# Kernel tuning notes

Measured on AMD Instinct MI355X. Metric: run time of the kernel, lower is better.

Reference implementation:

```python
import jax, jax.numpy as jnp
import numpy as np

N, E, R, H, FDIM, OUT = 50000, 800000, 12, 128, 1582, 2
Q = H // 4  # 32
SLOPE = 0.01  # LeakyReLU default negative slope


def leaky(x):
    return jnp.where(x > 0, x, SLOPE * x)


def rgcn(x, src, dst, etype, W, root, bias):
    # Per-relation mean aggregation of neighbor features, then linear transform
    # (PyG RGCNConv default aggr='mean'). Linear => transform-then-mean is equal.
    # count of edges of each (relation, dst) pair
    seg = etype * N + dst
    cnt = jnp.zeros((R * N,), x.dtype).at[seg].add(1.0)
    norm = 1.0 / jnp.maximum(cnt[seg], 1.0)          # [E]
    xw = jnp.einsum('nh,rhd->nrd', x, W)             # [N,R,H] per-relation transform
    msg = xw[src, etype] * norm[:, None]             # [E,H] gather + normalize
    agg = jax.ops.segment_sum(msg, dst, num_segments=N)  # [N,H] scatter-add
    return agg + x @ root + bias


def setup_inputs() -> dict:
    key = jax.random.key(0)
    ks = jax.random.split(key, 16)
    s = lambda d: 1.0 / np.sqrt(d)
    inp = {
        'feature': jax.random.normal(ks[0], (N, FDIM), jnp.float32),
        'edge_index': jax.random.randint(ks[1], (2, E), 0, N),
        'edge_type': jax.random.randint(ks[2], (E,), 0, R),
        'W_des': jax.random.normal(ks[3], (768, Q), jnp.float32) * s(768),
        'b_des': jnp.zeros((Q,), jnp.float32),
        'W_tweet': jax.random.normal(ks[4], (768, Q), jnp.float32) * s(768),
        'b_tweet': jnp.zeros((Q,), jnp.float32),
        'W_num': jax.random.normal(ks[5], (34, Q), jnp.float32) * s(34),
        'b_num': jnp.zeros((Q,), jnp.float32),
        'W_cat': jax.random.normal(ks[6], (12, Q), jnp.float32) * s(12),
        'b_cat': jnp.zeros((Q,), jnp.float32),
        'W_in': jax.random.normal(ks[7], (H, H), jnp.float32) * s(H),
        'b_in': jnp.zeros((H,), jnp.float32),
        'rgcn_W': jax.random.normal(ks[8], (R, H, H), jnp.float32) * s(H),
        'rgcn_root': jax.random.normal(ks[9], (H, H), jnp.float32) * s(H),
        'rgcn_bias': jnp.zeros((H,), jnp.float32),
        'W_out1': jax.random.normal(ks[10], (H, H), jnp.float32) * s(H),
        'b_out1': jnp.zeros((H,), jnp.float32),
        'W_out2': jax.random.normal(ks[11], (H, OUT), jnp.float32) * s(H),
        'b_out2': jnp.zeros((OUT,), jnp.float32),
    }
    return inp


def reference(feature, edge_index, edge_type, W_des, b_des, W_tweet, b_tweet,
              W_num, b_num, W_cat, b_cat, W_in, b_in, rgcn_W, rgcn_root,
              rgcn_bias, W_out1, b_out1, W_out2, b_out2):
    src, dst = edge_index[0], edge_index[1]
    d = leaky(feature[:, -1536:-768] @ W_des + b_des)
    t = leaky(feature[:, -768:] @ W_tweet + b_tweet)
    num = leaky(feature[:, 12:46] @ W_num + b_num)
    cat = leaky(feature[:, 0:12] @ W_cat + b_cat)
    x = jnp.concatenate((d, t, num, cat), axis=1)       # [N,H]
    x = leaky(x @ W_in + b_in)
    x = rgcn(x, src, dst, edge_type, rgcn_W, rgcn_root, rgcn_bias)
    # dropout: identity in eval mode (deterministic reference)
    x = rgcn(x, src, dst, edge_type, rgcn_W, rgcn_root, rgcn_bias)
    x = leaky(x @ W_out1 + b_out1)
    return x @ W_out2 + b_out2
```

## Files before the change

kernel.cpp:

```cpp
#include <hip/hip_runtime.h>
#include <stdint.h>

#define NN 50000
#define NE 800000
#define NR 12
#define NRX 13
#define NH 128
#define NF 1582
#define NSEG (NN * NR)
#define MT 3125
#define MT2 1563
#define SCAN_NB ((NSEG + 255) / 256)
#define KSENC 50
#define CTXW (NRX * 8)

typedef __attribute__((ext_vector_type(8))) short short8;
typedef __attribute__((ext_vector_type(4))) float floatx4;

__device__ __forceinline__ float bf2f(unsigned int u16) {
    union { unsigned int i; float f; } w; w.i = u16 << 16; return w.f;
}
__device__ __forceinline__ unsigned short f2bf(float f) {
    union { float f; unsigned int i; } w; w.f = f;
    unsigned int i = w.i;
    return (unsigned short)((i + 0x7FFFu + ((i >> 16) & 1u)) >> 16);
}
__device__ __forceinline__ float leaky_f(float v) { return v > 0.f ? v : 0.01f * v; }
__device__ __forceinline__ float fast_rcp(float x) {
    float r; asm("v_rcp_f32 %0, %1" : "=v"(r) : "v"(x)); return r;
}

__global__ __launch_bounds__(256) void swz_k(
    const float* __restrict__ src1, int K1,
    const float* __restrict__ src2, int Ktot, int N, int KS,
    unsigned short* __restrict__ dst)
{
    const int idx = blockIdx.x * 256 + threadIdx.x;
    const int total = (N >> 4) * KS * 512;
    if (idx >= total) return;
    const int j = idx & 7;
    const int lane = (idx >> 3) & 63;
    const int cks = idx >> 9;
    const int ks = cks % KS;
    const int ct = cks / KS;
    const int k = ks * 32 + (lane >> 4) * 8 + j;
    const int col = ct * 16 + (lane & 15);
    float v = 0.f;
    if (k < Ktot) v = (k < K1) ? src1[(size_t)k * N + col] : src2[(size_t)(k - K1) * N + col];
    dst[idx] = f2bf(v);
}

__global__ __launch_bounds__(256) void swzxw_k(
    const float* __restrict__ rgW, const float* __restrict__ root,
    unsigned short* __restrict__ dst)
{
    const int idx = blockIdx.x * 256 + threadIdx.x;
    const int total = CTXW * 4 * 512;
    if (idx >= total) return;
    const int j = idx & 7;
    const int lane = (idx >> 3) & 63;
    const int cks = idx >> 9;
    const int ks = cks & 3;
    const int ctg = cks >> 2;
    const int r = ctg >> 3;
    const int ct8 = ctg & 7;
    const int k = ks * 32 + (lane >> 4) * 8 + j;
    const int c = ct8 * 16 + (lane & 15);
    const float v = (r < NR) ? rgW[((size_t)r * NH + k) * NH + c]
                             : root[(size_t)k * NH + c];
    dst[idx] = f2bf(v);
}

__global__ __launch_bounds__(256) void swzenc_k(
    const float* __restrict__ Wdes, const float* __restrict__ Wtw,
    const float* __restrict__ Wnum, const float* __restrict__ Wcat,
    unsigned short* __restrict__ dst)
{
    const int idx = blockIdx.x * 256 + threadIdx.x;
    const int total = 8 * KSENC * 512;
    if (idx >= total) return;
    const int j = idx & 7;
    const int lane = (idx >> 3) & 63;
    const int cks = idx >> 9;
    const int ks = cks % KSENC;
    const int ct = cks / KSENC;
    const int k = ks * 32 + (lane >> 4) * 8 + j;
    const int col = ct * 16 + (lane & 15);
    float v = 0.f;
    if (col < 32) {
        if (k >= 46 && k < 814)   v = Wdes[(size_t)(k - 46) * 32 + col];
    } else if (col < 64) {
        if (k >= 814 && k < 1582) v = Wtw[(size_t)(k - 814) * 32 + (col - 32)];
    } else if (col < 96) {
        if (k >= 12 && k < 46)    v = Wnum[(size_t)(k - 12) * 32 + (col - 64)];
    } else {
        if (k < 12)               v = Wcat[(size_t)k * 32 + (col - 96)];
    }
    dst[idx] = f2bf(v);
}

__global__ __launch_bounds__(128) void packbias_k(
    const float* __restrict__ bdes, const float* __restrict__ btw,
    const float* __restrict__ bnum, const float* __restrict__ bcat,
    float* __restrict__ be)
{
    const int c = threadIdx.x;
    float v;
    if (c < 32) v = bdes[c];
    else if (c < 64) v = btw[c - 32];
    else if (c < 96) v = bnum[c - 64];
    else v = bcat[c - 96];
    be[c] = v;
}

__global__ __launch_bounds__(256) void hist_k(const int* __restrict__ dst,
                                              const int* __restrict__ et,
                                              int* __restrict__ deg)
{
    const int e = blockIdx.x * 256 + threadIdx.x;
    if (e >= NE) return;
    atomicAdd(&deg[dst[e] * NR + et[e]], 1);
}

__global__ __launch_bounds__(256) void scanA_k(const int* __restrict__ deg,
                                               int* __restrict__ offs,
                                               int* __restrict__ part)
{
    __shared__ int lds[256];
    const int i = blockIdx.x * 256 + threadIdx.x;
    const int v = (i < NSEG) ? deg[i] : 0;
    lds[threadIdx.x] = v; __syncthreads();
#pragma unroll
    for (int d = 1; d < 256; d <<= 1) {
        const int t = (threadIdx.x >= d) ? lds[threadIdx.x - d] : 0;
        __syncthreads();
        lds[threadIdx.x] += t;
        __syncthreads();
    }
    if (i < NSEG) offs[i] = lds[threadIdx.x] - v;
    if (threadIdx.x == 255) part[blockIdx.x] = lds[255];
}

__global__ __launch_bounds__(256) void scanB_k(int* __restrict__ part, int nb)
{
    __shared__ int lds[256];
    __shared__ int carry;
    if (threadIdx.x == 0) carry = 0;
    __syncthreads();
    for (int base = 0; base < nb; base += 256) {
        const int i = base + threadIdx.x;
        const int v = (i < nb) ? part[i] : 0;
        lds[threadIdx.x] = v; __syncthreads();
#pragma unroll
        for (int d = 1; d < 256; d <<= 1) {
            const int t = (threadIdx.x >= d) ? lds[threadIdx.x - d] : 0;
            __syncthreads();
            lds[threadIdx.x] += t;
            __syncthreads();
        }
        if (i < nb) part[i] = lds[threadIdx.x] - v + carry;
        __syncthreads();
        if (threadIdx.x == 255) carry += lds[255];
        __syncthreads();
    }
}

__global__ __launch_bounds__(256) void scanC_k(int* __restrict__ offs,
                                               const int* __restrict__ part)
{
    const int i = blockIdx.x * 256 + threadIdx.x;
    if (i < NSEG) offs[i] += part[blockIdx.x];
}

__global__ __launch_bounds__(256) void fill_k(const int* __restrict__ src,
                                              const int* __restrict__ dst,
                                              const int* __restrict__ et,
                                              const int* __restrict__ offs,
                                              const int* __restrict__ deg,
                                              int* __restrict__ cur,
                                              unsigned int* __restrict__ eidx)
{
    const int e = blockIdx.x * 256 + threadIdx.x;
    if (e >= NE) return;
    const int r = et[e];
    const int s = dst[e] * NR + r;
    const int pos = offs[s] + atomicAdd(&cur[s], 1);
    int n = deg[s]; if (n > 4095) n = 4095;
    eidx[pos] = (unsigned int)(src[e] * NRX + r) | ((unsigned int)n << 20);
}

__global__ __launch_bounds__(256) void enc_k(
    const float* __restrict__ feat,
    const unsigned short* __restrict__ Benc, const float* __restrict__ be,
    const unsigned short* __restrict__ Bwin, const float* __restrict__ bin,
    unsigned short* __restrict__ xa)
{
    const int wave = threadIdx.x >> 6, lane = threadIdx.x & 63;
    const int q = lane >> 4, cl = lane & 15;
    int tile = blockIdx.x * 4 + wave;
    if (tile >= MT) tile = MT - 1;
    const int row = tile * 16 + cl;

    const int lo[8] = {1, 1, 25, 25, 0, 0, 0, 0};
    const int hi[8] = {26, 26, 50, 50, 2, 2, 1, 1};

    floatx4 acc[8];
#pragma unroll
    for (int ct = 0; ct < 8; ct++) { floatx4 z = {0.f,0.f,0.f,0.f}; acc[ct] = z; }

    for (int ks = 0; ks < KSENC; ks++) {
        const int kb = ks * 32 + q * 8;
        union { short8 v; unsigned short u[8]; } a;
        const float* ap = feat + (size_t)row * NF + kb;
        if (kb + 7 < NF) {
#pragma unroll
            for (int j = 0; j < 4; j++) {
                const float2 t = *(const float2*)__builtin_assume_aligned(ap + 2 * j, 8);
                a.u[2 * j]     = f2bf(t.x);
                a.u[2 * j + 1] = f2bf(t.y);
            }
        } else {
#pragma unroll
            for (int j = 0; j < 8; j++)
                a.u[j] = ((kb + j) < NF) ? f2bf(ap[j]) : 0;
        }
#pragma unroll
        for (int ct = 0; ct < 8; ct++) {
            if (ks >= lo[ct] && ks < hi[ct]) {
                const short8 b = *(const short8*)(Benc + ((size_t)(ct * KSENC + ks) * 64 + lane) * 8);
                acc[ct] = __builtin_amdgcn_mfma_f32_16x16x32_bf16(a.v, b, acc[ct], 0, 0, 0);
            }
        }
    }

    __shared__ unsigned short lds[4][16][136];
#pragma unroll
    for (int ct = 0; ct < 8; ct++) {
        const int col = ct * 16 + cl;
        const float bv = be[col];
#pragma unroll
        for (int r = 0; r < 4; r++)
            lds[wave][q * 4 + r][col] = f2bf(leaky_f(acc[ct][r] + bv));
    }
    __syncthreads();

    floatx4 acc2[8];
#pragma unroll
    for (int ct = 0; ct < 8; ct++) { floatx4 z = {0.f,0.f,0.f,0.f}; acc2[ct] = z; }
#pragma unroll
    for (int ks2 = 0; ks2 < 4; ks2++) {
        const short8 a2 = *(const short8*)&lds[wave][cl][ks2 * 32 + q * 8];
#pragma unroll
        for (int ct = 0; ct < 8; ct++) {
            const short8 b = *(const short8*)(Bwin + ((size_t)(ct * 4 + ks2) * 64 + lane) * 8);
            acc2[ct] = __builtin_amdgcn_mfma_f32_16x16x32_bf16(a2, b, acc2[ct], 0, 0, 0);
        }
    }
#pragma unroll
    for (int ct = 0; ct < 8; ct++) {
        const int col = ct * 16 + cl;
        const float bv = bin[col];
#pragma unroll
        for (int r = 0; r < 4; r++)
            xa[(size_t)(tile * 16 + q * 4 + r) * NH + col] = f2bf(leaky_f(acc2[ct][r] + bv));
    }
}

__global__ __launch_bounds__(256) void xw_k(
    const unsigned short* __restrict__ xin,
    const unsigned short* __restrict__ Bxw,
    unsigned short* __restrict__ xw)
{
    const int wave = threadIdx.x >> 6, lane = threadIdx.x & 63;
    const int q = lane >> 4, cl = lane & 15;
    int wid = blockIdx.x * 4 + wave;
    if (wid >= MT2 * NRX) wid = MT2 * NRX - 1;
    __shared__ unsigned short tl[4][2][16][136];
    const int t2 = wid / NRX;
    const int r = wid - t2 * NRX;
    const int ta = t2 * 2;
    const int tb = (ta + 1 < MT) ? ta + 1 : MT - 1;

    floatx4 accA[8], accB[8];
#pragma unroll
    for (int ct = 0; ct < 8; ct++) {
        floatx4 z = {0.f,0.f,0.f,0.f}; accA[ct] = z; accB[ct] = z;
    }
#pragma unroll
    for (int ks = 0; ks < 4; ks++) {
        const short8 aA = *(const short8*)__builtin_assume_aligned(
            xin + (size_t)(ta * 16 + cl) * NH + ks * 32 + q * 8, 16);
        const short8 aB = *(const short8*)__builtin_assume_aligned(
            xin + (size_t)(tb * 16 + cl) * NH + ks * 32 + q * 8, 16);
#pragma unroll
        for (int ct = 0; ct < 8; ct++) {
            const short8 b = *(const short8*)(Bxw + ((size_t)((r * 8 + ct) * 4 + ks) * 64 + lane) * 8);
            accA[ct] = __builtin_amdgcn_mfma_f32_16x16x32_bf16(aA, b, accA[ct], 0, 0, 0);
            accB[ct] = __builtin_amdgcn_mfma_f32_16x16x32_bf16(aB, b, accB[ct], 0, 0, 0);
        }
    }
#pragma unroll
    for (int ct = 0; ct < 8; ct++) {
        const int col = ct * 16 + cl;
#pragma unroll
        for (int rr = 0; rr < 4; rr++) {
            tl[wave][0][q * 4 + rr][col] = f2bf(accA[ct][rr]);
            tl[wave][1][q * 4 + rr][col] = f2bf(accB[ct][rr]);
        }
    }
    __syncthreads();
#pragma unroll
    for (int i = 0; i < 4; i++) {
        const int row = i * 4 + q;
        const short8 vA = *(const short8*)&tl[wave][0][row][cl * 8];
        const short8 vB = *(const short8*)&tl[wave][1][row][cl * 8];
        *(short8*)(xw + ((size_t)(ta * 16 + row) * NRX + r) * NH + cl * 8) = vA;
        *(short8*)(xw + ((size_t)(tb * 16 + row) * NRX + r) * NH + cl * 8) = vB;
    }
}

#define ACC8(fk, tv, wv) \
    fk[0] += (wv) * bf2f((tv).x & 0xFFFFu); fk[1] += (wv) * bf2f((tv).x >> 16); \
    fk[2] += (wv) * bf2f((tv).y & 0xFFFFu); fk[3] += (wv) * bf2f((tv).y >> 16); \
    fk[4] += (wv) * bf2f((tv).z & 0xFFFFu); fk[5] += (wv) * bf2f((tv).z >> 16); \
    fk[6] += (wv) * bf2f((tv).w & 0xFFFFu); fk[7] += (wv) * bf2f((tv).w >> 16);

#define INIT8(fk, tv) \
    fk[0] = bf2f((tv).x & 0xFFFFu); fk[1] = bf2f((tv).x >> 16); \
    fk[2] = bf2f((tv).y & 0xFFFFu); fk[3] = bf2f((tv).y >> 16); \
    fk[4] = bf2f((tv).z & 0xFFFFu); fk[5] = bf2f((tv).z >> 16); \
    fk[6] = bf2f((tv).w & 0xFFFFu); fk[7] = bf2f((tv).w >> 16);

__global__ __launch_bounds__(256) void gather_k(
    const unsigned short* __restrict__ xw,
    const unsigned int* __restrict__ eidx,
    const int* __restrict__ offs,
    const float* __restrict__ rbias,
    unsigned short* __restrict__ xout)
{
    const int wave = threadIdx.x >> 6, lane = threadIdx.x & 63;
    const int q = lane >> 4, cl = lane & 15;
    const int wid = blockIdx.x * 4 + wave;
    const int tile = wid >> 1;
    if (tile >= MT) return;
    const int half = wid & 1;
    const int cA = half * 8 + q;
    const int cB = cA + 4;
    const int d = tile * 16 + cl;
    const int beg = offs[d * NR];
    const int end = (d < NN - 1) ? offs[(d + 1) * NR] : NE;

    float fA[8], fB[8];
    {
        const unsigned short* xr = xw + ((size_t)d * NRX + NR) * NH;
        const uint4 tA = *(const uint4*)(xr + cA * 8);
        const uint4 tB = *(const uint4*)(xr + cB * 8);
        INIT8(fA, tA); INIT8(fB, tB);
    }

    for (int e = beg; e < end; e += 2) {
        const int e1 = (e + 1 < end) ? e + 1 : e;
        const unsigned int v0 = eidx[e];
        const unsigned int v1 = eidx[e1];
        const float w0 = fast_rcp((float)(v0 >> 20));
        const float w1 = (e + 1 < end) ? fast_rcp((float)(v1 >> 20)) : 0.f;
        const unsigned short* x0 = xw + (size_t)(v0 & 0xFFFFFu) * NH;
        const unsigned short* x1 = xw + (size_t)(v1 & 0xFFFFFu) * NH;
        const uint4 a0 = *(const uint4*)(x0 + cA * 8);
        const uint4 b0 = *(const uint4*)(x0 + cB * 8);
        const uint4 a1 = *(const uint4*)(x1 + cA * 8);
        const uint4 b1 = *(const uint4*)(x1 + cB * 8);
        ACC8(fA, a0, w0); ACC8(fB, b0, w0);
        ACC8(fA, a1, w1); ACC8(fB, b1, w1);
    }

    union { short8 v; unsigned short u[8]; } oA, oB;
#pragma unroll
    for (int m = 0; m < 8; m++) {
        oA.u[m] = f2bf(fA[m] + rbias[cA * 8 + m]);
        oB.u[m] = f2bf(fB[m] + rbias[cB * 8 + m]);
    }
    *(short8*)(xout + (size_t)d * NH + cA * 8) = oA.v;
    *(short8*)(xout + (size_t)d * NH + cB * 8) = oB.v;
}

__global__ __launch_bounds__(256) void head_k(
    const unsigned short* __restrict__ xa,
    const unsigned short* __restrict__ Bo1, const float* __restrict__ bo1,
    const float* __restrict__ Wo2, const float* __restrict__ bo2,
    float* __restrict__ out)
{
    const int wave = threadIdx.x >> 6, lane = threadIdx.x & 63;
    const int q = lane >> 4, cl = lane & 15;
    int tile = blockIdx.x * 4 + wave;
    if (tile >= MT) tile = MT - 1;

    floatx4 acc[8];
#pragma unroll
    for (int ct = 0; ct < 8; ct++) { floatx4 z = {0.f,0.f,0.f,0.f}; acc[ct] = z; }
#pragma unroll
    for (int ks = 0; ks < 4; ks++) {
        const short8 a = *(const short8*)__builtin_assume_aligned(
            xa + (size_t)(tile * 16 + cl) * NH + ks * 32 + q * 8, 16);
#pragma unroll
        for (int ct = 0; ct < 8; ct++) {
            const short8 b = *(const short8*)(Bo1 + ((size_t)(ct * 4 + ks) * 64 + lane) * 8);
            acc[ct] = __builtin_amdgcn_mfma_f32_16x16x32_bf16(a, b, acc[ct], 0, 0, 0);
        }
    }
    __shared__ unsigned short lds[4][16][136];
#pragma unroll
    for (int ct = 0; ct < 8; ct++) {
        const int col = ct * 16 + cl;
        const float bv = bo1[col];
#pragma unroll
        for (int r = 0; r < 4; r++)
            lds[wave][q * 4 + r][col] = f2bf(leaky_f(acc[ct][r] + bv));
    }
    __syncthreads();

    if (lane < 32) {
        const int row = lane >> 1, o = lane & 1;
        float s = bo2[o];
        for (int k = 0; k < NH; k++)
            s += bf2f(lds[wave][row][k]) * Wo2[k * 2 + o];
        out[(size_t)(tile * 16 + row) * 2 + o] = s;
    }
}

extern "C" void kernel_launch(void* const* d_in, const int* in_sizes, int n_in,
                              void* d_out, int out_size, void* d_ws, size_t ws_size,
                              hipStream_t stream)
{
    const float* feat = (const float*)d_in[0];
    const int* ei   = (const int*)d_in[1];
    const int* et   = (const int*)d_in[2];
    const float* Wdes = (const float*)d_in[3];
    const float* bdes = (const float*)d_in[4];
    const float* Wtw  = (const float*)d_in[5];
    const float* btw  = (const float*)d_in[6];
    const float* Wnum = (const float*)d_in[7];
    const float* bnum = (const float*)d_in[8];
    const float* Wcat = (const float*)d_in[9];
    const float* bcat = (const float*)d_in[10];
    const float* Win  = (const float*)d_in[11];
    const float* bin  = (const float*)d_in[12];
    const float* rgW  = (const float*)d_in[13];
    const float* root = (const float*)d_in[14];
    const float* rbias= (const float*)d_in[15];
    const float* Wo1  = (const float*)d_in[16];
    const float* bo1  = (const float*)d_in[17];
    const float* Wo2  = (const float*)d_in[18];
    const float* bo2  = (const float*)d_in[19];
    const int* srcp = ei;
    const int* dstp = ei + NE;

    char* p = (char*)d_ws;
    auto alloc = [&](size_t bytes) { char* r = p; p += (bytes + 255) & ~(size_t)255; return r; };
    unsigned short* xa = (unsigned short*)alloc((size_t)NN * NH * 2);
    unsigned short* xb = (unsigned short*)alloc((size_t)NN * NH * 2);
    int* deg  = (int*)alloc((size_t)NSEG * 4);
    int* offs = (int*)alloc((size_t)NSEG * 4);
    int* cur  = (int*)alloc((size_t)NSEG * 4);
    int* part = (int*)alloc((size_t)(SCAN_NB + 8) * 4);
    unsigned int* eidx = (unsigned int*)alloc((size_t)NE * 4);
    unsigned short* Benc = (unsigned short*)alloc((size_t)8 * KSENC * 512 * 2);
    unsigned short* sWin = (unsigned short*)alloc((size_t)8 * 4 * 512 * 2);
    unsigned short* Bxw  = (unsigned short*)alloc((size_t)CTXW * 4 * 512 * 2);
    unsigned short* sWo1 = (unsigned short*)alloc((size_t)8 * 4 * 512 * 2);
    float* be = (float*)alloc(128 * 4);
    unsigned short* xwbuf = (unsigned short*)alloc((size_t)NN * NRX * NH * 2);

    const int GB = (MT + 3) / 4;
    const int GBXW = (MT2 * NRX + 3) / 4;
    const int GB2 = (MT * 2 + 3) / 4;

    hipMemsetAsync(deg, 0, (size_t)NSEG * 4, stream);
    hipMemsetAsync(cur, 0, (size_t)NSEG * 4, stream);
    hist_k<<<(NE + 255) / 256, 256, 0, stream>>>(dstp, et, deg);
    scanA_k<<<SCAN_NB, 256, 0, stream>>>(deg, offs, part);
    scanB_k<<<1, 256, 0, stream>>>(part, SCAN_NB);
    scanC_k<<<SCAN_NB, 256, 0, stream>>>(offs, part);
    fill_k<<<(NE + 255) / 256, 256, 0, stream>>>(srcp, dstp, et, offs, deg, cur, eidx);

    swzenc_k<<<(8 * KSENC * 512 + 255) / 256, 256, 0, stream>>>(Wdes, Wtw, Wnum, Wcat, Benc);
    packbias_k<<<1, 128, 0, stream>>>(bdes, btw, bnum, bcat, be);
    swz_k<<<(8 * 4 * 512 + 255) / 256, 256, 0, stream>>>(Win, 128, Win, 128, 128, 4, sWin);
    swzxw_k<<<(CTXW * 4 * 512 + 255) / 256, 256, 0, stream>>>(rgW, root, Bxw);
    swz_k<<<(8 * 4 * 512 + 255) / 256, 256, 0, stream>>>(Wo1, 128, Wo1, 128, 128, 4, sWo1);

    enc_k<<<GB, 256, 0, stream>>>(feat, Benc, be, sWin, bin, xa);
    xw_k<<<GBXW, 256, 0, stream>>>(xa, Bxw, xwbuf);
    gather_k<<<GB2, 256, 0, stream>>>(xwbuf, eidx, offs, rbias, xb);
    xw_k<<<GBXW, 256, 0, stream>>>(xb, Bxw, xwbuf);
    gather_k<<<GB2, 256, 0, stream>>>(xwbuf, eidx, offs, rbias, xa);
    head_k<<<GB, 256, 0, stream>>>(xa, sWo1, bo1, Wo2, bo2, (float*)d_out);
}
```

Measured before the change: 840.9 us.

## Merge prep kernels, drop scan fixup, fuse head into gather, unroll gather by four

Folds the weight-swizzle and bias-pack kernels into one prep kernel and replaces the memsets with a zero kernel. The scan fixup pass is removed; consumers add the block partial sum on the fly. The output head is fused into the second gather through shared memory, and the gather loop is unrolled to four edges per iteration for more memory-level parallelism. This cuts launch count and global round trips, at the cost of extra registers and a block-wide barrier in gather.

```diff
diff --git a/kernel.cpp b/kernel.cpp
--- a/kernel.cpp
+++ b/kernel.cpp
@@ -13,6 +13,10 @@
 #define SCAN_NB ((NSEG + 255) / 256)
 #define KSENC 50
 #define CTXW (NRX * 8)
+#define TOTENC (8 * KSENC * 512)
+#define TOT128 (8 * 4 * 512)
+#define TOTXW  (CTXW * 4 * 512)
+#define TOTPREP (TOTENC + TOT128 + TOTXW + TOT128 + 128)
 
 typedef __attribute__((ext_vector_type(8))) short short8;
 typedef __attribute__((ext_vector_type(4))) float floatx4;
@@ -30,87 +34,96 @@
     float r; asm("v_rcp_f32 %0, %1" : "=v"(r) : "v"(x)); return r;
 }
 
-__global__ __launch_bounds__(256) void swz_k(
-    const float* __restrict__ src1, int K1,
-    const float* __restrict__ src2, int Ktot, int N, int KS,
-    unsigned short* __restrict__ dst)
-{
-    const int idx = blockIdx.x * 256 + threadIdx.x;
-    const int total = (N >> 4) * KS * 512;
-    if (idx >= total) return;
-    const int j = idx & 7;
-    const int lane = (idx >> 3) & 63;
-    const int cks = idx >> 9;
-    const int ks = cks % KS;
-    const int ct = cks / KS;
-    const int k = ks * 32 + (lane >> 4) * 8 + j;
-    const int col = ct * 16 + (lane & 15);
-    float v = 0.f;
-    if (k < Ktot) v = (k < K1) ? src1[(size_t)k * N + col] : src2[(size_t)(k - K1) * N + col];
-    dst[idx] = f2bf(v);
-}
-
-__global__ __launch_bounds__(256) void swzxw_k(
-    const float* __restrict__ rgW, const float* __restrict__ root,
-    unsigned short* __restrict__ dst)
-{
-    const int idx = blockIdx.x * 256 + threadIdx.x;
-    const int total = CTXW * 4 * 512;
-    if (idx >= total) return;
-    const int j = idx & 7;
-    const int lane = (idx >> 3) & 63;
-    const int cks = idx >> 9;
-    const int ks = cks & 3;
-    const int ctg = cks >> 2;
-    const int r = ctg >> 3;
-    const int ct8 = ctg & 7;
-    const int k = ks * 32 + (lane >> 4) * 8 + j;
-    const int c = ct8 * 16 + (lane & 15);
-    const float v = (r < NR) ? rgW[((size_t)r * NH + k) * NH + c]
-                             : root[(size_t)k * NH + c];
-    dst[idx] = f2bf(v);
-}
-
-__global__ __launch_bounds__(256) void swzenc_k(
+__global__ __launch_bounds__(256) void prep_k(
     const float* __restrict__ Wdes, const float* __restrict__ Wtw,
     const float* __restrict__ Wnum, const float* __restrict__ Wcat,
-    unsigned short* __restrict__ dst)
-{
-    const int idx = blockIdx.x * 256 + threadIdx.x;
-    const int total = 8 * KSENC * 512;
-    if (idx >= total) return;
-    const int j = idx & 7;
-    const int lane = (idx >> 3) & 63;
-    const int cks = idx >> 9;
-    const int ks = cks % KSENC;
-    const int ct = cks / KSENC;
-    const int k = ks * 32 + (lane >> 4) * 8 + j;
-    const int col = ct * 16 + (lane & 15);
-    float v = 0.f;
-    if (col < 32) {
-        if (k >= 46 && k < 814)   v = Wdes[(size_t)(k - 46) * 32 + col];
-    } else if (col < 64) {
-        if (k >= 814 && k < 1582) v = Wtw[(size_t)(k - 814) * 32 + (col - 32)];
-    } else if (col < 96) {
-        if (k >= 12 && k < 46)    v = Wnum[(size_t)(k - 12) * 32 + (col - 64)];
-    } else {
-        if (k < 12)               v = Wcat[(size_t)k * 32 + (col - 96)];
-    }
-    dst[idx] = f2bf(v);
-}
-
-__global__ __launch_bounds__(128) void packbias_k(
+    const float* __restrict__ Win,  const float* __restrict__ rgW,
+    const float* __restrict__ root, const float* __restrict__ Wo1,
     const float* __restrict__ bdes, const float* __restrict__ btw,
     const float* __restrict__ bnum, const float* __restrict__ bcat,
+    unsigned short* __restrict__ Benc, unsigned short* __restrict__ sWin,
+    unsigned short* __restrict__ Bxw,  unsigned short* __restrict__ sWo1,
     float* __restrict__ be)
 {
-    const int c = threadIdx.x;
-    float v;
-    if (c < 32) v = bdes[c];
-    else if (c < 64) v = btw[c - 32];
-    else if (c < 96) v = bnum[c - 64];
-    else v = bcat[c - 96];
-    be[c] = v;
+    int idx = blockIdx.x * 256 + threadIdx.x;
+    if (idx < TOTENC) {
+        const int j = idx & 7;
+        const int lane = (idx >> 3) & 63;
+        const int cks = idx >> 9;
+        const int ks = cks % KSENC;
+        const int ct = cks / KSENC;
+        const int k = ks * 32 + (lane >> 4) * 8 + j;
+        const int col = ct * 16 + (lane & 15);
+        float v = 0.f;
+        if (col < 32) {
+            if (k >= 46 && k < 814)   v = Wdes[(size_t)(k - 46) * 32 + col];
+        } else if (col < 64) {
+            if (k >= 814 && k < 1582) v = Wtw[(size_t)(k - 814) * 32 + (col - 32)];
+        } else if (col < 96) {
+            if (k >= 12 && k < 46)    v = Wnum[(size_t)(k - 12) * 32 + (col - 64)];
+        } else {
+            if (k < 12)               v = Wcat[(size_t)k * 32 + (col - 96)];
+        }
+        Benc[idx] = f2bf(v);
+        return;
+    }
+    idx -= TOTENC;
+    if (idx < TOT128) {
+        const int j = idx & 7;
+        const int lane = (idx >> 3) & 63;
+        const int cks = idx >> 9;
+        const int ks = cks & 3;
+        const int ct = cks >> 2;
+        const int k = ks * 32 + (lane >> 4) * 8 + j;
+        const int col = ct * 16 + (lane & 15);
+        sWin[idx] = f2bf(Win[(size_t)k * NH + col]);
+        return;
+    }
+    idx -= TOT128;
+    if (idx < TOTXW) {
+        const int j = idx & 7;
+        const int lane = (idx >> 3) & 63;
+        const int cks = idx >> 9;
+        const int ks = cks & 3;
+        const int ctg = cks >> 2;
+        const int r = ctg >> 3;
+        const int ct8 = ctg & 7;
+        const int k = ks * 32 + (lane >> 4) * 8 + j;
+        const int c = ct8 * 16 + (lane & 15);
+        const float v = (r < NR) ? rgW[((size_t)r * NH + k) * NH + c]
+                                 : root[(size_t)k * NH + c];
+        Bxw[idx] = f2bf(v);
+        return;
+    }
+    idx -= TOTXW;
+    if (idx < TOT128) {
+        const int j = idx & 7;
+        const int lane = (idx >> 3) & 63;
+        const int cks = idx >> 9;
+        const int ks = cks & 3;
+        const int ct = cks >> 2;
+        const int k = ks * 32 + (lane >> 4) * 8 + j;
+        const int col = ct * 16 + (lane & 15);
+        sWo1[idx] = f2bf(Wo1[(size_t)k * NH + col]);
+        return;
+    }
+    idx -= TOT128;
+    if (idx < 128) {
+        const int c = idx;
+        float v;
+        if (c < 32) v = bdes[c];
+        else if (c < 64) v = btw[c - 32];
+        else if (c < 96) v = bnum[c - 64];
+        else v = bcat[c - 96];
+        be[c] = v;
+    }
+}
+
+__global__ __launch_bounds__(256) void zero_k(int* __restrict__ deg,
+                                              int* __restrict__ cur)
+{
+    const int i = blockIdx.x * 256 + threadIdx.x;
+    if (i < NSEG) { deg[i] = 0; cur[i] = 0; }
 }
 
 __global__ __launch_bounds__(256) void hist_k(const int* __restrict__ dst,
@@ -165,17 +178,11 @@
     }
 }
 
-__global__ __launch_bounds__(256) void scanC_k(int* __restrict__ offs,
-                                               const int* __restrict__ part)
-{
-    const int i = blockIdx.x * 256 + threadIdx.x;
-    if (i < NSEG) offs[i] += part[blockIdx.x];
-}
-
 __global__ __launch_bounds__(256) void fill_k(const int* __restrict__ src,
                                               const int* __restrict__ dst,
                                               const int* __restrict__ et,
                                               const int* __restrict__ offs,
+                                              const int* __restrict__ part,
                                               const int* __restrict__ deg,
                                               int* __restrict__ cur,
                                               unsigned int* __restrict__ eidx)
@@ -184,7 +191,7 @@
     if (e >= NE) return;
     const int r = et[e];
     const int s = dst[e] * NR + r;
-    const int pos = offs[s] + atomicAdd(&cur[s], 1);
+    const int pos = offs[s] + part[s >> 8] + atomicAdd(&cur[s], 1);
     int n = deg[s]; if (n > 4095) n = 4095;
     eidx[pos] = (unsigned int)(src[e] * NRX + r) | ((unsigned int)n << 20);
 }
@@ -334,21 +341,31 @@
 __global__ __launch_bounds__(256) void gather_k(
     const unsigned short* __restrict__ xw,
     const unsigned int* __restrict__ eidx,
-    const int* __restrict__ offs,
+    const int* __restrict__ offs, const int* __restrict__ part,
     const float* __restrict__ rbias,
-    unsigned short* __restrict__ xout)
+    unsigned short* __restrict__ xout,
+    const int do_head,
+    const unsigned short* __restrict__ Bo1, const float* __restrict__ bo1,
+    const float* __restrict__ Wo2, const float* __restrict__ bo2,
+    float* __restrict__ out)
 {
     const int wave = threadIdx.x >> 6, lane = threadIdx.x & 63;
     const int q = lane >> 4, cl = lane & 15;
-    const int wid = blockIdx.x * 4 + wave;
+    int wid = blockIdx.x * 4 + wave;
+    if (wid >= MT * 2) wid = MT * 2 - 1;
     const int tile = wid >> 1;
-    if (tile >= MT) return;
     const int half = wid & 1;
+    const int lt = wave >> 1;
+    __shared__ unsigned short lx[2][16][136];
+
     const int cA = half * 8 + q;
     const int cB = cA + 4;
     const int d = tile * 16 + cl;
-    const int beg = offs[d * NR];
-    const int end = (d < NN - 1) ? offs[(d + 1) * NR] : NE;
+    const int s0 = d * NR;
+    const int beg = offs[s0] + part[s0 >> 8];
+    int end;
+    if (d < NN - 1) { const int s1 = s0 + NR; end = offs[s1] + part[s1 >> 8]; }
+    else end = NE;
 
     float fA[8], fB[8];
     {
@@ -358,20 +375,34 @@
         INIT8(fA, tA); INIT8(fB, tB);
     }
 
-    for (int e = beg; e < end; e += 2) {
+    for (int e = beg; e < end; e += 4) {
         const int e1 = (e + 1 < end) ? e + 1 : e;
+        const int e2 = (e + 2 < end) ? e + 2 : e;
+        const int e3 = (e + 3 < end) ? e + 3 : e;
         const unsigned int v0 = eidx[e];
         const unsigned int v1 = eidx[e1];
+        const unsigned int v2 = eidx[e2];
+        const unsigned int v3 = eidx[e3];
         const float w0 = fast_rcp((float)(v0 >> 20));
         const float w1 = (e + 1 < end) ? fast_rcp((float)(v1 >> 20)) : 0.f;
+        const float w2 = (e + 2 < end) ? fast_rcp((float)(v2 >> 20)) : 0.f;
+        const float w3 = (e + 3 < end) ? fast_rcp((float)(v3 >> 20)) : 0.f;
         const unsigned short* x0 = xw + (size_t)(v0 & 0xFFFFFu) * NH;
         const unsigned short* x1 = xw + (size_t)(v1 & 0xFFFFFu) * NH;
+        const unsigned short* x2 = xw + (size_t)(v2 & 0xFFFFFu) * NH;
+        const unsigned short* x3 = xw + (size_t)(v3 & 0xFFFFFu) * NH;
         const uint4 a0 = *(const uint4*)(x0 + cA * 8);
         const uint4 b0 = *(const uint4*)(x0 + cB * 8);
         const uint4 a1 = *(const uint4*)(x1 + cA * 8);
         const uint4 b1 = *(const uint4*)(x1 + cB * 8);
+        const uint4 a2 = *(const uint4*)(x2 + cA * 8);
+        const uint4 b2 = *(const uint4*)(x2 + cB * 8);
+        const uint4 a3 = *(const uint4*)(x3 + cA * 8);
+        const uint4 b3 = *(const uint4*)(x3 + cB * 8);
         ACC8(fA, a0, w0); ACC8(fB, b0, w0);
         ACC8(fA, a1, w1); ACC8(fB, b1, w1);
+        ACC8(fA, a2, w2); ACC8(fB, b2, w2);
+        ACC8(fA, a3, w3); ACC8(fB, b3, w3);
     }
 
     union { short8 v; unsigned short u[8]; } oA, oB;
@@ -380,51 +411,44 @@
         oA.u[m] = f2bf(fA[m] + rbias[cA * 8 + m]);
         oB.u[m] = f2bf(fB[m] + rbias[cB * 8 + m]);
     }
-    *(short8*)(xout + (size_t)d * NH + cA * 8) = oA.v;
-    *(short8*)(xout + (size_t)d * NH + cB * 8) = oB.v;
-}
-
-__global__ __launch_bounds__(256) void head_k(
-    const unsigned short* __restrict__ xa,
-    const unsigned short* __restrict__ Bo1, const float* __restrict__ bo1,
-    const float* __restrict__ Wo2, const float* __restrict__ bo2,
-    float* __restrict__ out)
-{
-    const int wave = threadIdx.x >> 6, lane = threadIdx.x & 63;
-    const int q = lane >> 4, cl = lane & 15;
-    int tile = blockIdx.x * 4 + wave;
-    if (tile >= MT) tile = MT - 1;
-
-    floatx4 acc[8];
-#pragma unroll
-    for (int ct = 0; ct < 8; ct++) { floatx4 z = {0.f,0.f,0.f,0.f}; acc[ct] = z; }
-#pragma unroll
-    for (int ks = 0; ks < 4; ks++) {
-        const short8 a = *(const short8*)__builtin_assume_aligned(
-            xa + (size_t)(tile * 16 + cl) * NH + ks * 32 + q * 8, 16);
+
+    if (!do_head) {
+        *(short8*)(xout + (size_t)d * NH + cA * 8) = oA.v;
+        *(short8*)(xout + (size_t)d * NH + cB * 8) = oB.v;
+        return;
+    }
+
+    *(short8*)&lx[lt][cl][cA * 8] = oA.v;
+    *(short8*)&lx[lt][cl][cB * 8] = oB.v;
+    __syncthreads();
+    if (half == 0) {
+        floatx4 acc[8];
+#pragma unroll
+        for (int ct = 0; ct < 8; ct++) { floatx4 z = {0.f,0.f,0.f,0.f}; acc[ct] = z; }
+#pragma unroll
+        for (int ks = 0; ks < 4; ks++) {
+            const short8 a = *(const short8*)&lx[lt][cl][ks * 32 + q * 8];
+#pragma unroll
+            for (int ct = 0; ct < 8; ct++) {
+                const short8 b = *(const short8*)(Bo1 + ((size_t)(ct * 4 + ks) * 64 + lane) * 8);
+                acc[ct] = __builtin_amdgcn_mfma_f32_16x16x32_bf16(a, b, acc[ct], 0, 0, 0);
+            }
+        }
 #pragma unroll
         for (int ct = 0; ct < 8; ct++) {
-            const short8 b = *(const short8*)(Bo1 + ((size_t)(ct * 4 + ks) * 64 + lane) * 8);
-            acc[ct] = __builtin_amdgcn_mfma_f32_16x16x32_bf16(a, b, acc[ct], 0, 0, 0);
-        }
-    }
-    __shared__ unsigned short lds[4][16][136];
-#pragma unroll
-    for (int ct = 0; ct < 8; ct++) {
-        const int col = ct * 16 + cl;
-        const float bv = bo1[col];
-#pragma unroll
-        for (int r = 0; r < 4; r++)
-            lds[wave][q * 4 + r][col] = f2bf(leaky_f(acc[ct][r] + bv));
-    }
-    __syncthreads();
-
-    if (lane < 32) {
-        const int row = lane >> 1, o = lane & 1;
-        float s = bo2[o];
-        for (int k = 0; k < NH; k++)
-            s += bf2f(lds[wave][row][k]) * Wo2[k * 2 + o];
-        out[(size_t)(tile * 16 + row) * 2 + o] = s;
+            const int col = ct * 16 + cl;
+            const float bv = bo1[col];
+#pragma unroll
+            for (int r2 = 0; r2 < 4; r2++)
+                lx[lt][q * 4 + r2][col] = f2bf(leaky_f(acc[ct][r2] + bv));
+        }
+        if (lane < 32) {
+            const int row = lane >> 1, o = lane & 1;
+            float s = bo2[o];
+            for (int k = 0; k < NH; k++)
+                s += bf2f(lx[lt][row][k]) * Wo2[k * 2 + o];
+            out[(size_t)(tile * 16 + row) * 2 + o] = s;
+        }
     }
 }
 
@@ -464,10 +488,10 @@
     int* cur  = (int*)alloc((size_t)NSEG * 4);
     int* part = (int*)alloc((size_t)(SCAN_NB + 8) * 4);
     unsigned int* eidx = (unsigned int*)alloc((size_t)NE * 4);
-    unsigned short* Benc = (unsigned short*)alloc((size_t)8 * KSENC * 512 * 2);
-    unsigned short* sWin = (unsigned short*)alloc((size_t)8 * 4 * 512 * 2);
-    unsigned short* Bxw  = (unsigned short*)alloc((size_t)CTXW * 4 * 512 * 2);
-    unsigned short* sWo1 = (unsigned short*)alloc((size_t)8 * 4 * 512 * 2);
+    unsigned short* Benc = (unsigned short*)alloc((size_t)TOTENC * 2);
+    unsigned short* sWin = (unsigned short*)alloc((size_t)TOT128 * 2);
+    unsigned short* Bxw  = (unsigned short*)alloc((size_t)TOTXW * 2);
+    unsigned short* sWo1 = (unsigned short*)alloc((size_t)TOT128 * 2);
     float* be = (float*)alloc(128 * 4);
     unsigned short* xwbuf = (unsigned short*)alloc((size_t)NN * NRX * NH * 2);
 
@@ -475,24 +499,21 @@
     const int GBXW = (MT2 * NRX + 3) / 4;
     const int GB2 = (MT * 2 + 3) / 4;
 
-    hipMemsetAsync(deg, 0, (size_t)NSEG * 4, stream);
-    hipMemsetAsync(cur, 0, (size_t)NSEG * 4, stream);
+    zero_k<<<SCAN_NB, 256, 0, stream>>>(deg, cur);
     hist_k<<<(NE + 255) / 256, 256, 0, stream>>>(dstp, et, deg);
     scanA_k<<<SCAN_NB, 256, 0, stream>>>(deg, offs, part);
     scanB_k<<<1, 256, 0, stream>>>(part, SCAN_NB);
-    scanC_k<<<SCAN_NB, 256, 0, stream>>>(offs, part);
-    fill_k<<<(NE + 255) / 256, 256, 0, stream>>>(srcp, dstp, et, offs, deg, cur, eidx);
-
-    swzenc_k<<<(8 * KSENC * 512 + 255) / 256, 256, 0, stream>>>(Wdes, Wtw, Wnum, Wcat, Benc);
-    packbias_k<<<1, 128, 0, stream>>>(bdes, btw, bnum, bcat, be);
-    swz_k<<<(8 * 4 * 512 + 255) / 256, 256, 0, stream>>>(Win, 128, Win, 128, 128, 4, sWin);
-    swzxw_k<<<(CTXW * 4 * 512 + 255) / 256, 256, 0, stream>>>(rgW, root, Bxw);
-    swz_k<<<(8 * 4 * 512 + 255) / 256, 256, 0, stream>>>(Wo1, 128, Wo1, 128, 128, 4, sWo1);
+    fill_k<<<(NE + 255) / 256, 256, 0, stream>>>(srcp, dstp, et, offs, part, deg, cur, eidx);
+
+    prep_k<<<(TOTPREP + 255) / 256, 256, 0, stream>>>(
+        Wdes, Wtw, Wnum, Wcat, Win, rgW, root, Wo1,
+        bdes, btw, bnum, bcat, Benc, sWin, Bxw, sWo1, be);
 
     enc_k<<<GB, 256, 0, stream>>>(feat, Benc, be, sWin, bin, xa);
     xw_k<<<GBXW, 256, 0, stream>>>(xa, Bxw, xwbuf);
-    gather_k<<<GB2, 256, 0, stream>>>(xwbuf, eidx, offs, rbias, xb);
+    gather_k<<<GB2, 256, 0, stream>>>(xwbuf, eidx, offs, part, rbias, xb, 0,
+                                      sWo1, bo1, Wo2, bo2, (float*)d_out);
     xw_k<<<GBXW, 256, 0, stream>>>(xb, Bxw, xwbuf);
-    gather_k<<<GB2, 256, 0, stream>>>(xwbuf, eidx, offs, rbias, xa);
-    head_k<<<GB, 256, 0, stream>>>(xa, sWo1, bo1, Wo2, bo2, (float*)d_out);
-}
+    gather_k<<<GB2, 256, 0, stream>>>(xwbuf, eidx, offs, part, rbias, xa, 1,
+                                      sWo1, bo1, Wo2, bo2, (float*)d_out);
+}
```

Result: no change. 825.4 us (-1.8%).
